# Kernel tuning notes

Measured on AMD Instinct MI355X. Metric: run time of the kernel, lower is better.

## Reference

```python
import jax, jax.numpy as jnp
import numpy as np

T, NTOK, D = 8, 32768, 128
N_ENTIRE, COMP_LEN, COMP_DIM = 65536, 8, 64


def _layer_norm(v, w, b, eps=1e-5):
    m = v.mean(-1, keepdims=True)
    c = v - m
    var = (c * c).mean(-1, keepdims=True)
    return c * jax.lax.rsqrt(var + eps) * w + b


def setup_inputs() -> dict:
    key = jax.random.key(0)
    ks = jax.random.split(key, 8)
    x = jax.random.normal(ks[0], (T, NTOK, D), jnp.float32)
    padded_node_mask = jnp.ones((T, NTOK), dtype=bool)  # all tokens are nodes
    # unique per-timestamp scatter indices into the 'entire node' axis
    node_idx = jax.vmap(lambda k: jax.random.permutation(k, N_ENTIRE)[:NTOK])(
        jax.random.split(ks[1], T)).astype(jnp.int32)
    s = 0.02
    return dict(
        x=x,
        ln1_w=jnp.ones((D,), jnp.float32), ln1_b=jnp.zeros((D,), jnp.float32),
        w1=jax.random.normal(ks[2], (D, 2 * COMP_DIM), jnp.float32) * s,
        b1=jnp.zeros((2 * COMP_DIM,), jnp.float32),
        w2=jax.random.normal(ks[3], (2 * COMP_DIM, COMP_DIM), jnp.float32) * s,
        b2=jnp.zeros((COMP_DIM,), jnp.float32),
        lnf_w=jnp.ones((COMP_LEN * COMP_DIM,), jnp.float32),
        lnf_b=jnp.zeros((COMP_LEN * COMP_DIM,), jnp.float32),
        padded_node_mask=padded_node_mask,
        node_idx=node_idx,
        n_entire=N_ENTIRE,
    )


def reference(x, ln1_w, ln1_b, w1, b1, w2, b2, lnf_w, lnf_b,
              padded_node_mask, node_idx, n_entire):
    t, ntok, d = x.shape
    # encode_layer_norm over all tokens
    xn = _layer_norm(x, ln1_w, ln1_b)
    # nodes = xn[padded_node_mask].reshape(t, ntok, d); mask is all-True here
    nodes = jnp.where(padded_node_mask[..., None], xn, 0.0)
    # scga._to_entire: scatter nodes into [t, n_entire, d] (zeros elsewhere)
    tenodes = jnp.zeros((t, n_entire, d), x.dtype)
    tenodes = tenodes.at[jnp.arange(t)[:, None], node_idx].set(nodes)
    # eval mode: np.array_split(arange(n_entire), comp_len) = equal contiguous groups
    g = n_entire // COMP_LEN
    xg = tenodes.reshape(t, COMP_LEN, g, d)  # [t, L, g, d]
    # per-group MLP (Linear->GELU->(Dropout=id)->Linear) then mean over group
    h = jax.nn.gelu(jnp.einsum('tlgd,de->tlge', xg, w1) + b1, approximate=False)
    c = jnp.einsum('tlge,ec->tlgc', h, w2) + b2
    comp = c.mean(axis=2)  # [t, L, comp_dim]
    compressed = _layer_norm(comp.reshape(t, 1, COMP_LEN * COMP_DIM), lnf_w, lnf_b)
    # orthogonality loss over the L compressed components (exact torch pair loop)
    f = comp.transpose(1, 0, 2).reshape(COMP_LEN, -1)  # [L, t*comp_dim]
    fn = f / jnp.linalg.norm(f, axis=-1, keepdims=True)
    dots = []
    for i in range(COMP_LEN - 1):
        for j in range(1, COMP_LEN):
            dots.append(jnp.sum(fn[i] * fn[j]) / jnp.sum(fn[i] + fn[j]))
    ortho_loss = jnp.mean(jnp.stack(dots) ** 2)
    return compressed, ortho_loss
```

## Files before the change

### kernel.cpp

```cpp
#include <hip/hip_runtime.h>
#include <math.h>

#define TT 8
#define NTOK 32768
#define DD 128
#define LCOMP 8
#define GSZ 8192
#define CDIM 64
#define EDIM 128
#define NPART 8

#define BATCH 16
#define BPW 8
#define WAVES 4
#define TOKBLK (WAVES*BPW*BATCH)
#define NBLK (TT*NTOK/TOKBLK)

#define O_CZERO 0
#define O_W2BT  256
#define O_W1BT  (256 + EDIM*CDIM*2)
#define O_CSUMP (O_W1BT + DD*EDIM*2)

typedef __attribute__((ext_vector_type(8))) short bf16x8;
typedef __attribute__((ext_vector_type(4))) float f32x4;

__device__ __forceinline__ ushort f2bf(float f) {
    union { float f; uint u; } c; c.f = f;
    uint u = c.u;
    return (ushort)((u + 0x7FFFu + ((u >> 16) & 1u)) >> 16);
}

__device__ __forceinline__ float gelu_f(float a) {
    float x = a * 0.70710678118654752f;
    float ax = fabsf(x);
    float t = 1.0f / (1.0f + 0.3275911f * ax);
    float p = t * (0.254829592f + t * (-0.284496736f + t * (1.421413741f +
              t * (-1.453152027f + t * 1.061405429f))));
    float e = __expf(-x * x);
    float er = copysignf(1.0f - p * e, x);
    return 0.5f * a * (1.0f + er);
}

__global__ void prep_kernel(const float* __restrict__ w1, const float* __restrict__ b1,
                            const float* __restrict__ w2,
                            ushort* __restrict__ w1bt, ushort* __restrict__ w2bt,
                            float* __restrict__ czero, float* __restrict__ csum_p) {
    int gid = blockIdx.x * 256 + threadIdx.x;
    if (gid < DD * EDIM) {
        int j = gid >> 7, d = gid & 127;
        w1bt[j * 128 + d] = f2bf(w1[d * EDIM + j]);
    }
    if (gid < EDIM * CDIM) {
        int k = gid >> 7, jj = gid & 127;
        w2bt[k * 128 + jj] = f2bf(w2[jj * CDIM + k]);
    }
    if (gid < CDIM) {
        float a2 = 0.f;
        for (int dd = 0; dd < EDIM; ++dd)
            a2 += gelu_f(b1[dd]) * w2[dd * CDIM + gid];
        czero[gid] = a2;
    }
#pragma unroll
    for (int i = 0; i < 2; ++i)
        csum_p[gid + i * 16384] = 0.f;
}

__global__ __launch_bounds__(256, 2)
void main_kernel(const float* __restrict__ x,
                 const float* __restrict__ ln1w, const float* __restrict__ ln1b,
                 const float* __restrict__ b1g,
                 const ushort* __restrict__ w1bt, const ushort* __restrict__ w2bt,
                 const float* __restrict__ czero,
                 const int* __restrict__ node_idx,
                 float* __restrict__ csum_p) {
    __shared__ ushort s_h[WAVES * 2048];
    __shared__ float  s_acc[LCOMP * 65];

    const int tid = threadIdx.x;
    const int w   = tid >> 6;
    const int ln  = tid & 63;
    const int cs  = ln >> 4;
    const int tk  = ln & 15;
    const int bid = blockIdx.x;

    for (int idx = tid; idx < LCOMP * 65; idx += 256) s_acc[idx] = 0.f;

    bf16x8 w1f[8][4];
#pragma unroll
    for (int jt = 0; jt < 8; ++jt)
#pragma unroll
        for (int ks = 0; ks < 4; ++ks)
            w1f[jt][ks] = *(const bf16x8*)(w1bt + (jt*16 + tk)*128 + ks*32 + cs*8);
    bf16x8 w2f[4][4];
#pragma unroll
    for (int kt = 0; kt < 4; ++kt)
#pragma unroll
        for (int ks = 0; ks < 4; ++ks)
            w2f[kt][ks] = *(const bf16x8*)(w2bt + (kt*16 + tk)*128 + ks*32 + cs*8);

    __syncthreads();

    const size_t wbase = (size_t)bid * TOKBLK + w * (BPW * BATCH);
    char* hbase = (char*)s_h + w * 4096;

    float v[32];
    {
        const float* xp = x + (wbase + tk) * (size_t)DD + cs * 8;
#pragma unroll
        for (int m = 0; m < 4; ++m) {
            float4 a = *(const float4*)(xp + m*32);
            float4 b = *(const float4*)(xp + m*32 + 4);
            v[m*8+0]=a.x; v[m*8+1]=a.y; v[m*8+2]=a.z; v[m*8+3]=a.w;
            v[m*8+4]=b.x; v[m*8+5]=b.y; v[m*8+6]=b.z; v[m*8+7]=b.w;
        }
    }

    for (int b = 0; b < BPW; ++b) {
        const size_t tb = wbase + (size_t)b * BATCH;
        const int lg = node_idx[tb + tk] >> 13;

        float s = 0.f, q = 0.f;
#pragma unroll
        for (int i = 0; i < 32; ++i) { s += v[i]; q += v[i]*v[i]; }
        s += __shfl_xor(s, 16, 64); q += __shfl_xor(q, 16, 64);
        s += __shfl_xor(s, 32, 64); q += __shfl_xor(q, 32, 64);
        float mean = s * (1.f/128.f);
        float var  = q * (1.f/128.f) - mean*mean;
        float rs   = rsqrtf(var + 1e-5f);

        bf16x8 xnf[4];
#pragma unroll
        for (int m = 0; m < 4; ++m) {
            const float* lwp = ln1w + m*32 + cs*8;
            const float* lbp = ln1b + m*32 + cs*8;
            float4 lw0 = *(const float4*)(lwp),   lw1 = *(const float4*)(lwp + 4);
            float4 lb0 = *(const float4*)(lbp),   lb1 = *(const float4*)(lbp + 4);
            float g0 = (v[m*8+0]-mean)*rs*lw0.x + lb0.x;
            float g1 = (v[m*8+1]-mean)*rs*lw0.y + lb0.y;
            float g2 = (v[m*8+2]-mean)*rs*lw0.z + lb0.z;
            float g3 = (v[m*8+3]-mean)*rs*lw0.w + lb0.w;
            float g4 = (v[m*8+4]-mean)*rs*lw1.x + lb1.x;
            float g5 = (v[m*8+5]-mean)*rs*lw1.y + lb1.y;
            float g6 = (v[m*8+6]-mean)*rs*lw1.z + lb1.z;
            float g7 = (v[m*8+7]-mean)*rs*lw1.w + lb1.w;
            uint4 pk;
            pk.x = f2bf(g0) | ((uint)f2bf(g1) << 16);
            pk.y = f2bf(g2) | ((uint)f2bf(g3) << 16);
            pk.z = f2bf(g4) | ((uint)f2bf(g5) << 16);
            pk.w = f2bf(g6) | ((uint)f2bf(g7) << 16);
            xnf[m] = __builtin_bit_cast(bf16x8, pk);
        }

        if (b + 1 < BPW) {
            const float* xq = x + (tb + BATCH + tk) * (size_t)DD + cs * 8;
#pragma unroll
            for (int m = 0; m < 4; ++m) {
                float4 a = *(const float4*)(xq + m*32);
                float4 bb = *(const float4*)(xq + m*32 + 4);
                v[m*8+0]=a.x;  v[m*8+1]=a.y;  v[m*8+2]=a.z;  v[m*8+3]=a.w;
                v[m*8+4]=bb.x; v[m*8+5]=bb.y; v[m*8+6]=bb.z; v[m*8+7]=bb.w;
            }
        }

        f32x4 acc1[8];
#pragma unroll
        for (int jt = 0; jt < 8; ++jt) acc1[jt] = (f32x4){0.f,0.f,0.f,0.f};
#pragma unroll
        for (int ks = 0; ks < 4; ++ks)
#pragma unroll
            for (int jt = 0; jt < 8; ++jt)
                acc1[jt] = __builtin_amdgcn_mfma_f32_16x16x32_bf16(
                    w1f[jt][ks], xnf[ks], acc1[jt], 0, 0, 0);

#pragma unroll
        for (int jt = 0; jt < 8; ++jt) {
            float g0 = gelu_f(acc1[jt][0] + b1g[jt*16 + cs*4 + 0]);
            float g1 = gelu_f(acc1[jt][1] + b1g[jt*16 + cs*4 + 1]);
            float g2 = gelu_f(acc1[jt][2] + b1g[jt*16 + cs*4 + 2]);
            float g3 = gelu_f(acc1[jt][3] + b1g[jt*16 + cs*4 + 3]);
            uint2 pk2;
            pk2.x = f2bf(g0) | ((uint)f2bf(g1) << 16);
            pk2.y = f2bf(g2) | ((uint)f2bf(g3) << 16);
            int c16 = (jt*2 + (cs >> 1)) ^ tk;
            *(uint2*)(hbase + tk*256 + c16*16 + (cs & 1)*8) = pk2;
        }
        bf16x8 B2[4];
#pragma unroll
        for (int ks = 0; ks < 4; ++ks) {
            int c16 = (ks*4 + cs) ^ tk;
            B2[ks] = *(const bf16x8*)(hbase + tk*256 + c16*16);
        }

        f32x4 acc2[4];
#pragma unroll
        for (int kt = 0; kt < 4; ++kt) acc2[kt] = (f32x4){0.f,0.f,0.f,0.f};
#pragma unroll
        for (int ks = 0; ks < 4; ++ks)
#pragma unroll
            for (int kt = 0; kt < 4; ++kt)
                acc2[kt] = __builtin_amdgcn_mfma_f32_16x16x32_bf16(
                    w2f[kt][ks], B2[ks], acc2[kt], 0, 0, 0);

#pragma unroll
        for (int kt = 0; kt < 4; ++kt)
#pragma unroll
            for (int r = 0; r < 4; ++r)
                atomicAdd(&s_acc[lg*65 + kt*16 + cs*4 + r],
                          acc2[kt][r] - czero[kt*16 + cs*4 + r]);
    }

    __syncthreads();

    {
        int t8 = (bid >> 6) * LCOMP;
        int p  = bid & (NPART - 1);
        for (int idx = tid; idx < LCOMP * CDIM; idx += 256) {
            int l = idx >> 6, k = idx & 63;
            atomicAdd(&csum_p[(p * 64 + t8 + l) * 64 + k], s_acc[l*65 + k]);
        }
    }
}

__global__ void fin_kernel(const float* __restrict__ csum_p, const float* __restrict__ czero,
                           const float* __restrict__ b2,
                           const float* __restrict__ lnfw, const float* __restrict__ lnfb,
                           float* __restrict__ out) {
    __shared__ float comp[TT * LCOMP * CDIM];
    __shared__ float norm_s[LCOMP], sum_s[LCOMP], red[8];
    int tid = threadIdx.x;

    for (int idx = tid; idx < TT * LCOMP * CDIM; idx += 512) {
        int bin = idx >> 6, k = idx & 63;
        float s = 0.f;
        for (int p = 0; p < NPART; ++p) s += csum_p[(p * 64 + bin) * 64 + k];
        comp[idx] = s * (1.f / GSZ) + czero[k] + b2[k];
    }
    __syncthreads();

    int wave = tid >> 6, lane = tid & 63;

    {
        int t = wave;
        float s = 0.f, q = 0.f;
        for (int e = lane; e < 512; e += 64) {
            float v = comp[t * 512 + e];
            s += v; q += v * v;
        }
#pragma unroll
        for (int off = 32; off > 0; off >>= 1) {
            s += __shfl_xor(s, off, 64);
            q += __shfl_xor(q, off, 64);
        }
        float m = s * (1.f / 512.f);
        float var = q * (1.f / 512.f) - m * m;
        float rs = rsqrtf(var + 1e-5f);
        for (int e = lane; e < 512; e += 64) {
            float v = comp[t * 512 + e];
            out[t * 512 + e] = (v - m) * rs * lnfw[e] + lnfb[e];
        }
    }

    {
        int l = wave;
        float s2 = 0.f, s1 = 0.f;
        for (int qd = lane; qd < 512; qd += 64) {
            int t = qd >> 6, k = qd & 63;
            float v = comp[t * 512 + l * 64 + k];
            s2 += v * v; s1 += v;
        }
#pragma unroll
        for (int off = 32; off > 0; off >>= 1) {
            s2 += __shfl_xor(s2, off, 64);
            s1 += __shfl_xor(s1, off, 64);
        }
        if (lane == 0) { norm_s[l] = sqrtf(s2); sum_s[l] = s1; }
    }
    __syncthreads();

    float loss_part = 0.f;
    for (int p = wave; p < 49; p += 8) {
        int i = p / 7, j = 1 + p % 7;
        float d = 0.f;
        for (int qd = lane; qd < 512; qd += 64) {
            int t = qd >> 6, k = qd & 63;
            d += comp[t * 512 + i * 64 + k] * comp[t * 512 + j * 64 + k];
        }
#pragma unroll
        for (int off = 32; off > 0; off >>= 1) d += __shfl_xor(d, off, 64);
        float ni = norm_s[i], nj = norm_s[j];
        float dot = (d / (ni * nj)) / (sum_s[i] / ni + sum_s[j] / nj);
        loss_part += dot * dot;
    }
    if (lane == 0) red[wave] = loss_part;
    __syncthreads();
    if (tid == 0) {
        float tot = 0.f;
        for (int w2_ = 0; w2_ < 8; ++w2_) tot += red[w2_];
        out[4096] = tot * (1.f / 49.f);
    }
}

extern "C" void kernel_launch(void* const* d_in, const int* in_sizes, int n_in,
                              void* d_out, int out_size, void* d_ws, size_t ws_size,
                              hipStream_t stream) {
    const float* x    = (const float*)d_in[0];
    const float* ln1w = (const float*)d_in[1];
    const float* ln1b = (const float*)d_in[2];
    const float* w1   = (const float*)d_in[3];
    const float* b1   = (const float*)d_in[4];
    const float* w2   = (const float*)d_in[5];
    const float* b2   = (const float*)d_in[6];
    const float* lnfw = (const float*)d_in[7];
    const float* lnfb = (const float*)d_in[8];
    const int* node_idx = (const int*)d_in[10];
    float* out = (float*)d_out;

    char* wsb = (char*)d_ws;
    float*  czero  = (float*)(wsb + O_CZERO);
    ushort* w2bt   = (ushort*)(wsb + O_W2BT);
    ushort* w1bt   = (ushort*)(wsb + O_W1BT);
    float*  csum_p = (float*)(wsb + O_CSUMP);

    prep_kernel<<<64, 256, 0, stream>>>(w1, b1, w2, w1bt, w2bt, czero, csum_p);
    main_kernel<<<NBLK, 256, 0, stream>>>(x, ln1w, ln1b, b1, w1bt, w2bt, czero,
                                          node_idx, csum_p);
    fin_kernel<<<1, 512, 0, stream>>>(csum_p, czero, b2, lnfw, lnfb, out);
}
```

Baseline: 380.2 us.

## Stage MLP weights in XOR-swizzled LDS instead of holding them in registers

The bf16 W1/W2 fragments move from per-thread registers (48 bf16x8 vectors) into shared memory. Each block copies them in once, and the MFMA loops reload them from LDS on every batch. The prep kernel writes the weights with an XOR swizzle on 16-byte slots so the LDS reads avoid bank conflicts. The aim is to free registers, but it adds 48KB of LDS per block, which may limit occupancy, plus extra LDS traffic inside the inner loop.

```diff
diff --git a/kernel.cpp b/kernel.cpp
--- a/kernel.cpp
+++ b/kernel.cpp
@@ -48,11 +48,13 @@
     int gid = blockIdx.x * 256 + threadIdx.x;
     if (gid < DD * EDIM) {
         int j = gid >> 7, d = gid & 127;
-        w1bt[j * 128 + d] = f2bf(w1[d * EDIM + j]);
+        int slot = (d >> 3) ^ (j & 7);
+        w1bt[j * 128 + slot * 8 + (d & 7)] = f2bf(w1[d * EDIM + j]);
     }
     if (gid < EDIM * CDIM) {
         int k = gid >> 7, jj = gid & 127;
-        w2bt[k * 128 + jj] = f2bf(w2[jj * CDIM + k]);
+        int slot = (jj >> 3) ^ (k & 7);
+        w2bt[k * 128 + slot * 8 + (jj & 7)] = f2bf(w2[jj * CDIM + k]);
     }
     if (gid < CDIM) {
         float a2 = 0.f;
@@ -73,6 +75,8 @@
                  const float* __restrict__ czero,
                  const int* __restrict__ node_idx,
                  float* __restrict__ csum_p) {
+    __shared__ ushort s_w1[DD * EDIM];
+    __shared__ ushort s_w2[CDIM * EDIM];
     __shared__ ushort s_h[WAVES * 2048];
     __shared__ float  s_acc[LCOMP * 65];
 
@@ -81,24 +85,21 @@
     const int ln  = tid & 63;
     const int cs  = ln >> 4;
     const int tk  = ln & 15;
+    const int t7  = tk & 7;
     const int bid = blockIdx.x;
 
     for (int idx = tid; idx < LCOMP * 65; idx += 256) s_acc[idx] = 0.f;
 
-    bf16x8 w1f[8][4];
-#pragma unroll
-    for (int jt = 0; jt < 8; ++jt)
-#pragma unroll
-        for (int ks = 0; ks < 4; ++ks)
-            w1f[jt][ks] = *(const bf16x8*)(w1bt + (jt*16 + tk)*128 + ks*32 + cs*8);
-    bf16x8 w2f[4][4];
-#pragma unroll
-    for (int kt = 0; kt < 4; ++kt)
-#pragma unroll
-        for (int ks = 0; ks < 4; ++ks)
-            w2f[kt][ks] = *(const bf16x8*)(w2bt + (kt*16 + tk)*128 + ks*32 + cs*8);
-
-    __syncthreads();
+    {
+        const uint4* g1 = (const uint4*)w1bt;
+        const uint4* g2 = (const uint4*)w2bt;
+        uint4* l1 = (uint4*)s_w1;
+        uint4* l2 = (uint4*)s_w2;
+#pragma unroll
+        for (int i = 0; i < 8; ++i) l1[tid + i * 256] = g1[tid + i * 256];
+#pragma unroll
+        for (int i = 0; i < 4; ++i) l2[tid + i * 256] = g2[tid + i * 256];
+    }
 
     const size_t wbase = (size_t)bid * TOKBLK + w * (BPW * BATCH);
     char* hbase = (char*)s_h + w * 4096;
@@ -114,6 +115,8 @@
             v[m*8+4]=b.x; v[m*8+5]=b.y; v[m*8+6]=b.z; v[m*8+7]=b.w;
         }
     }
+
+    __syncthreads();
 
     for (int b = 0; b < BPW; ++b) {
         const size_t tb = wbase + (size_t)b * BATCH;
@@ -166,11 +169,17 @@
 #pragma unroll
         for (int jt = 0; jt < 8; ++jt) acc1[jt] = (f32x4){0.f,0.f,0.f,0.f};
 #pragma unroll
-        for (int ks = 0; ks < 4; ++ks)
-#pragma unroll
-            for (int jt = 0; jt < 8; ++jt)
-                acc1[jt] = __builtin_amdgcn_mfma_f32_16x16x32_bf16(
-                    w1f[jt][ks], xnf[ks], acc1[jt], 0, 0, 0);
+        for (int jt = 0; jt < 8; ++jt) {
+            const char* wrow = (const char*)s_w1 + (jt*16 + tk) * 256;
+            bf16x8 f0 = *(const bf16x8*)(wrow + ((0*4 + cs) ^ t7) * 16);
+            bf16x8 f1 = *(const bf16x8*)(wrow + ((1*4 + cs) ^ t7) * 16);
+            bf16x8 f2 = *(const bf16x8*)(wrow + ((2*4 + cs) ^ t7) * 16);
+            bf16x8 f3 = *(const bf16x8*)(wrow + ((3*4 + cs) ^ t7) * 16);
+            acc1[jt] = __builtin_amdgcn_mfma_f32_16x16x32_bf16(f0, xnf[0], acc1[jt], 0, 0, 0);
+            acc1[jt] = __builtin_amdgcn_mfma_f32_16x16x32_bf16(f1, xnf[1], acc1[jt], 0, 0, 0);
+            acc1[jt] = __builtin_amdgcn_mfma_f32_16x16x32_bf16(f2, xnf[2], acc1[jt], 0, 0, 0);
+            acc1[jt] = __builtin_amdgcn_mfma_f32_16x16x32_bf16(f3, xnf[3], acc1[jt], 0, 0, 0);
+        }
 
 #pragma unroll
         for (int jt = 0; jt < 8; ++jt) {
@@ -195,11 +204,17 @@
 #pragma unroll
         for (int kt = 0; kt < 4; ++kt) acc2[kt] = (f32x4){0.f,0.f,0.f,0.f};
 #pragma unroll
-        for (int ks = 0; ks < 4; ++ks)
-#pragma unroll
-            for (int kt = 0; kt < 4; ++kt)
-                acc2[kt] = __builtin_amdgcn_mfma_f32_16x16x32_bf16(
-                    w2f[kt][ks], B2[ks], acc2[kt], 0, 0, 0);
+        for (int kt = 0; kt < 4; ++kt) {
+            const char* wrow = (const char*)s_w2 + (kt*16 + tk) * 256;
+            bf16x8 f0 = *(const bf16x8*)(wrow + ((0*4 + cs) ^ t7) * 16);
+            bf16x8 f1 = *(const bf16x8*)(wrow + ((1*4 + cs) ^ t7) * 16);
+            bf16x8 f2 = *(const bf16x8*)(wrow + ((2*4 + cs) ^ t7) * 16);
+            bf16x8 f3 = *(const bf16x8*)(wrow + ((3*4 + cs) ^ t7) * 16);
+            acc2[kt] = __builtin_amdgcn_mfma_f32_16x16x32_bf16(f0, B2[0], acc2[kt], 0, 0, 0);
+            acc2[kt] = __builtin_amdgcn_mfma_f32_16x16x32_bf16(f1, B2[1], acc2[kt], 0, 0, 0);
+            acc2[kt] = __builtin_amdgcn_mfma_f32_16x16x32_bf16(f2, B2[2], acc2[kt], 0, 0, 0);
+            acc2[kt] = __builtin_amdgcn_mfma_f32_16x16x32_bf16(f3, B2[3], acc2[kt], 0, 0, 0);
+        }
 
 #pragma unroll
         for (int kt = 0; kt < 4; ++kt)
```

After: 381.8 us. Within noise of the previous version (+0.4%).
